# Kernel tuning notes

Hardware: AMD Instinct MI355X
Metric: run time of the kernel (lower is better)

The kernel has to match this reference:

```python
import jax, jax.numpy as jnp
import numpy as np
from jax import lax

B_, L_, D_ = 4, 2048, 256
DI, NS, DC, DTR = 512, 16, 4, 16  # d_inner=2*D, d_state, d_conv, dt_rank=ceil(D/16)
DFF = 4 * D_


def setup_inputs():
    key = jax.random.key(0)
    ks = jax.random.split(key, 20)
    rn = lambda k, s, sc=0.02: jax.random.normal(k, s, jnp.float32) * sc
    return {
        "x": jax.random.normal(ks[0], (B_, L_, D_), jnp.float32),
        "in_proj_w": rn(ks[1], (2 * DI, D_)), "in_proj_b": jnp.zeros((2 * DI,), jnp.float32),
        "conv_w": rn(ks[2], (DI, DC), 0.1), "conv_b": jnp.zeros((DI,), jnp.float32),
        "x_proj_w": rn(ks[3], (DTR + 2 * NS, DI)),
        "dt_proj_w": rn(ks[4], (DI, DTR), 0.1), "dt_proj_b": rn(ks[5], (DI,), 0.5),
        "A_log": jnp.log(jnp.tile(jnp.arange(1, NS + 1, dtype=jnp.float32), (DI, 1))),
        "D_ssm": jnp.ones((DI,), jnp.float32),
        "out_proj_w": rn(ks[6], (D_, DI)), "out_proj_b": jnp.zeros((D_,), jnp.float32),
        "ln1_g": jnp.ones((D_,), jnp.float32), "ln1_b": jnp.zeros((D_,), jnp.float32),
        "fc1_w": rn(ks[7], (DFF, D_)), "fc1_b": jnp.zeros((DFF,), jnp.float32),
        "fc2_w": rn(ks[8], (D_, DFF)), "fc2_b": jnp.zeros((D_,), jnp.float32),
        "ln2_g": jnp.ones((D_,), jnp.float32), "ln2_b": jnp.zeros((D_,), jnp.float32),
    }


def _layer_norm(x, g, b, eps=1e-5):
    m = jnp.mean(x, -1, keepdims=True)
    v = jnp.mean((x - m) ** 2, -1, keepdims=True)
    return (x - m) / jnp.sqrt(v + eps) * g + b


def _mamba(x, in_proj_w, in_proj_b, conv_w, conv_b, x_proj_w, dt_proj_w, dt_proj_b, A_log, D_ssm, out_proj_w, out_proj_b):
    B, L, D = x.shape
    xz = x @ in_proj_w.T + in_proj_b                       # [B,L,2*DI]
    xi, z = jnp.split(xz, 2, axis=-1)
    # causal depthwise conv over time
    xc = jnp.transpose(xi, (0, 2, 1))                       # [B,DI,L]
    xc = lax.conv_general_dilated(xc, conv_w[:, None, :], (1,), [(DC - 1, 0)],
                                  dimension_numbers=("NCH", "OIH", "NCH"),
                                  feature_group_count=DI)
    xi = jax.nn.silu(jnp.transpose(xc + conv_b[None, :, None], (0, 2, 1)))  # [B,L,DI]
    x_dbl = xi @ x_proj_w.T                                 # [B,L,DTR+2*NS]
    dt, Bs, Cs = jnp.split(x_dbl, [DTR, DTR + NS], axis=-1)
    dt = jax.nn.softplus(dt @ dt_proj_w.T + dt_proj_b)      # [B,L,DI]
    A = -jnp.exp(A_log)                                     # [DI,NS]
    dA = jnp.exp(dt[..., None] * A)                         # [B,L,DI,NS]
    dBu = dt[..., None] * Bs[:, :, None, :] * xi[..., None]  # [B,L,DI,NS]
    dA_t = jnp.moveaxis(dA, 1, 0)
    dBu_t = jnp.moveaxis(dBu, 1, 0)
    C_t = jnp.moveaxis(Cs, 1, 0)                            # [L,B,NS]

    def step(h, inp):
        a, bu, c = inp
        h = a * h + bu                                      # [B,DI,NS]
        y = jnp.einsum("bdn,bn->bd", h, c)
        return h, y

    h0 = jnp.zeros((B, DI, NS), x.dtype)
    _, ys = lax.scan(step, h0, (dA_t, dBu_t, C_t))
    y = jnp.moveaxis(ys, 0, 1) + xi * D_ssm                 # [B,L,DI]
    y = y * jax.nn.silu(z)
    return y @ out_proj_w.T + out_proj_b


def reference(x, in_proj_w, in_proj_b, conv_w, conv_b, x_proj_w, dt_proj_w, dt_proj_b,
              A_log, D_ssm, out_proj_w, out_proj_b, ln1_g, ln1_b, fc1_w, fc1_b,
              fc2_w, fc2_b, ln2_g, ln2_b):
    gelu = lambda t: jax.nn.gelu(t, approximate=False)
    ssm = _mamba(x, in_proj_w, in_proj_b, conv_w, conv_b, x_proj_w, dt_proj_w,
                 dt_proj_b, A_log, D_ssm, out_proj_w, out_proj_b)
    y = _layer_norm(x + ssm, ln1_g, ln1_b)                  # dropout = identity (eval)
    ffn = gelu(gelu(y @ fc1_w.T + fc1_b) @ fc2_w.T + fc2_b)
    return _layer_norm(y + ffn, ln2_g, ln2_b)
```

## Files before the change

kernel.cpp:

```cpp
#include <hip/hip_runtime.h>

typedef __bf16 bf16x8 __attribute__((ext_vector_type(8)));
typedef float  f32x4  __attribute__((ext_vector_type(4)));

#define AS1 __attribute__((address_space(1)))
#define AS3 __attribute__((address_space(3)))

__device__ __forceinline__ float bf2f(ushort u) {
    union { unsigned int i; float f; } v; v.i = ((unsigned int)u) << 16; return v.f;
}
__device__ __forceinline__ ushort f2bf(float f) {
    union { float f; unsigned int i; } v; v.f = f;
    unsigned int i = v.i;
    unsigned int r = i + 0x7FFFu + ((i >> 16) & 1u);
    return (ushort)(r >> 16);
}
__device__ __forceinline__ float bflo(unsigned int u) { return bf2f((ushort)(u & 0xFFFFu)); }
__device__ __forceinline__ float bfhi(unsigned int u) { return bf2f((ushort)(u >> 16)); }
__device__ __forceinline__ float gelu_f(float v) {
    return 0.5f * v * (1.f + erff(v * 0.70710678118654752f));
}

__device__ __forceinline__ bool sniff_inline(const ushort* __restrict__ x) {
    const int lane = threadIdx.x & 63;
    int cnt = 0;
    #pragma unroll
    for (int r = 0; r < 4; r++) {
        const ushort u = x[lane + r * 64];
        const int e = (u >> 7) & 0xFF;
        if ((u & 0x7FFF) == 0 || (e >= 112 && e <= 141)) cnt++;
    }
    #pragma unroll
    for (int o = 32; o > 0; o >>= 1) cnt += __shfl_xor(cnt, o);
    return cnt >= 224;
}

struct CanonArgs {
    const void* src[20];
    int off[20];
    int total;
};

__launch_bounds__(256)
__global__ void canon_k(CanonArgs a, ushort* __restrict__ dst, ushort* __restrict__ xpw_pad,
                        const ushort* __restrict__ sniffx)
{
    const int i = blockIdx.x * 256 + threadIdx.x;
    if (i >= a.total) {
        const int j = i - a.total;
        if (j < 8192) xpw_pad[24576 + j] = 0;
        return;
    }
    const bool fl = sniff_inline(sniffx);
    int s = 0;
    #pragma unroll
    for (int t = 1; t < 20; t++) if (i >= a.off[t]) s = t;
    const int li = i - a.off[s];
    ushort v;
    if (fl) v = ((const ushort*)a.src[s])[li];
    else    v = f2bf(((const float*)a.src[s])[li]);
    dst[i] = v;
    if (s == 5) xpw_pad[li] = v;
}

template<int BM, int BN>
__launch_bounds__(256, 2)
__global__ void gemm_bt(const ushort* __restrict__ A, const ushort* __restrict__ W,
                        const ushort* __restrict__ bias, ushort* __restrict__ Cb,
                        int N, int K)
{
    constexpr int WMT = BM / 32;
    constexpr int WNT = BN / 32;
    __shared__ __align__(16) ushort As[BM * 32];
    __shared__ __align__(16) ushort Bs[BN * 32];
    const int tid  = threadIdx.x;
    const int wave = tid >> 6;
    const int lane = tid & 63;
    const int m0 = blockIdx.x * BM;
    const int n0 = blockIdx.y * BN;
    const int wm = (wave >> 1) * (BM / 2);
    const int wn = (wave & 1) * (BN / 2);
    const int lrow = lane & 15;
    const int quad = lane >> 4;

    f32x4 acc[WMT][WNT];
    #pragma unroll
    for (int i = 0; i < WMT; i++)
        #pragma unroll
        for (int j = 0; j < WNT; j++)
            #pragma unroll
            for (int r = 0; r < 4; r++) acc[i][j][r] = 0.f;

    for (int k0 = 0; k0 < K; k0 += 32) {
        #pragma unroll
        for (int t = 0; t < BM / 64; t++) {
            const int inst = t * 4 + wave;
            const int row  = inst * 16 + (lane >> 2);
            const int sub  = lane & 3;
            const ushort* gp = A + (size_t)(m0 + row) * K + (k0 + sub * 8);
            __builtin_amdgcn_global_load_lds((AS1 void*)(void*)gp,
                                             (AS3 void*)(As + inst * 512), 16, 0, 0);
        }
        #pragma unroll
        for (int t = 0; t < BN / 64; t++) {
            const int inst = t * 4 + wave;
            const int row  = inst * 16 + (lane >> 2);
            const int sub  = lane & 3;
            const ushort* gp = W + (size_t)(n0 + row) * K + (k0 + sub * 8);
            __builtin_amdgcn_global_load_lds((AS1 void*)(void*)gp,
                                             (AS3 void*)(Bs + inst * 512), 16, 0, 0);
        }
        __syncthreads();
        bf16x8 afr[WMT], bfr[WNT];
        #pragma unroll
        for (int i = 0; i < WMT; i++)
            afr[i] = *(const bf16x8*)&As[(wm + i * 16 + lrow) * 32 + quad * 8];
        #pragma unroll
        for (int j = 0; j < WNT; j++)
            bfr[j] = *(const bf16x8*)&Bs[(wn + j * 16 + lrow) * 32 + quad * 8];
        #pragma unroll
        for (int i = 0; i < WMT; i++)
            #pragma unroll
            for (int j = 0; j < WNT; j++)
                acc[i][j] = __builtin_amdgcn_mfma_f32_16x16x32_bf16(afr[i], bfr[j], acc[i][j], 0, 0, 0);
        __syncthreads();
    }

    #pragma unroll
    for (int i = 0; i < WMT; i++) {
        const int gm = m0 + wm + i * 16 + quad * 4;
        #pragma unroll
        for (int j = 0; j < WNT; j++) {
            const int gn = n0 + wn + j * 16 + lrow;
            const float bv = bf2f(bias[gn]);
            #pragma unroll
            for (int r = 0; r < 4; r++)
                Cb[(size_t)(gm + r) * N + gn] = f2bf(acc[i][j][r] + bv);
        }
    }
}

__launch_bounds__(512)
__global__ void convscan1_k(const ushort* __restrict__ xz, const ushort* __restrict__ cw,
                            const ushort* __restrict__ cb, const ushort* __restrict__ xpw_pad,
                            const ushort* __restrict__ dtw, const ushort* __restrict__ dtb,
                            const ushort* __restrict__ Alog,
                            float* __restrict__ xdbl, float* __restrict__ summh,
                            float* __restrict__ sdtb)
{
    __shared__ __align__(16) ushort xcs[16 * 520];
    __shared__ float XD[16 * 48];
    const int tid  = threadIdx.x;
    const int wave = tid >> 6;
    const int lane = tid & 63;
    const int lrow = lane & 15;
    const int quad = lane >> 4;
    const int c = blockIdx.x, b = blockIdx.y;
    const int t0 = b * 2048 + c * 16;

    {
        const int d8 = (tid & 63) * 8;
        ushort wl[32];
        *(uint4*)&wl[0]  = *(const uint4*)&cw[d8 * 4];
        *(uint4*)&wl[8]  = *(const uint4*)&cw[d8 * 4 + 8];
        *(uint4*)&wl[16] = *(const uint4*)&cw[d8 * 4 + 16];
        *(uint4*)&wl[24] = *(const uint4*)&cw[d8 * 4 + 24];
        ushort bl[8];
        *(uint4*)&bl[0] = *(const uint4*)&cb[d8];
        #pragma unroll
        for (int it = 0; it < 2; it++) {
            const int trow = it * 8 + wave;
            const int t = t0 + trow;
            const int l = t & 2047;
            float acc[8];
            #pragma unroll
            for (int j = 0; j < 8; j++) acc[j] = bf2f(bl[j]);
            #pragma unroll
            for (int k = 0; k < 4; k++) {
                const int ls = l - 3 + k;
                if (ls >= 0) {
                    ushort xl[8];
                    *(uint4*)&xl[0] = *(const uint4*)&xz[(size_t)(t - 3 + k) * 1024 + d8];
                    #pragma unroll
                    for (int j = 0; j < 8; j++) acc[j] += bf2f(xl[j]) * bf2f(wl[j * 4 + k]);
                }
            }
            ushort ol[8];
            #pragma unroll
            for (int j = 0; j < 8; j++) {
                const float s = acc[j] / (1.f + __expf(-acc[j]));
                ol[j] = f2bf(s);
            }
            *(uint4*)&xcs[trow * 520 + d8] = *(uint4*)&ol[0];
        }
    }
    __syncthreads();

    if (wave < 3) {
        const int nt = wave;
        const ushort* bptr = xpw_pad + (size_t)(nt * 16 + lrow) * 512 + quad * 8;
        f32x4 acc = {0.f, 0.f, 0.f, 0.f};
        bf16x8 bn = *(const bf16x8*)bptr;
        for (int k0 = 0; k0 < 512; k0 += 32) {
            const bf16x8 bc = bn;
            if (k0 + 32 < 512) bn = *(const bf16x8*)(bptr + k0 + 32);
            const bf16x8 afr = *(const bf16x8*)&xcs[lrow * 520 + k0 + quad * 8];
            acc = __builtin_amdgcn_mfma_f32_16x16x32_bf16(afr, bc, acc, 0, 0, 0);
        }
        const int col = nt * 16 + lrow;
        #pragma unroll
        for (int r = 0; r < 4; r++) {
            const int row = quad * 4 + r;
            XD[row * 48 + col] = acc[r];
            xdbl[(size_t)(t0 + row) * 64 + col] = acc[r];
        }
    }
    __syncthreads();

    {
        const int d = tid;
        const uint4 w0 = *(const uint4*)&dtw[d * 16];
        const uint4 w1 = *(const uint4*)&dtw[d * 16 + 8];
        const float wd[16] = { bflo(w0.x), bfhi(w0.x), bflo(w0.y), bfhi(w0.y),
                               bflo(w0.z), bfhi(w0.z), bflo(w0.w), bfhi(w0.w),
                               bflo(w1.x), bfhi(w1.x), bflo(w1.y), bfhi(w1.y),
                               bflo(w1.z), bfhi(w1.z), bflo(w1.w), bfhi(w1.w) };
        const float dtbv = bf2f(dtb[d]);
        float A[16], h[16];
        #pragma unroll
        for (int n = 0; n < 16; n++) {
            A[n] = -__expf(bf2f(Alog[d * 16 + n]));
            h[n] = 0.f;
        }
        float sdt = 0.f;
        for (int i = 0; i < 16; i++) {
            const float* Xr = &XD[i * 48];
            float s = dtbv;
            #pragma unroll
            for (int k = 0; k < 16; k++) s += Xr[k] * wd[k];
            const float dtv = (s > 15.f) ? s : __logf(1.f + __expf(s));
            const float xiv = bf2f(xcs[i * 520 + d]);
            const float dx = dtv * xiv;
            sdt += dtv;
            #pragma unroll
            for (int n = 0; n < 16; n++) {
                const float da = __expf(dtv * A[n]);
                h[n] = da * h[n] + dx * Xr[16 + n];
            }
        }
        const size_t bh = ((size_t)(b * 128 + c) * 16) * 512 + d;
        #pragma unroll
        for (int n = 0; n < 16; n++) summh[bh + (size_t)n * 512] = h[n];
        sdtb[(size_t)(b * 128 + c) * 512 + d] = sdt;
    }
}

__launch_bounds__(512)
__global__ void combine_k(float* __restrict__ summh, const float* __restrict__ sdtb,
                          const ushort* __restrict__ Alog)
{
    const int b = blockIdx.x >> 4, n = blockIdx.x & 15;
    const int d = threadIdx.x;
    const float An = -__expf(bf2f(Alog[d * 16 + n]));
    float h = 0.f;
    #pragma unroll
    for (int q = 0; q < 4; q++) {
        float p[32], hl[32], ho[32];
        #pragma unroll
        for (int c2 = 0; c2 < 32; c2++) {
            const int cc = q * 32 + c2;
            hl[c2] = summh[((size_t)(b * 128 + cc) * 16 + n) * 512 + d];
            p[c2]  = __expf(An * sdtb[(size_t)(b * 128 + cc) * 512 + d]);
        }
        #pragma unroll
        for (int c2 = 0; c2 < 32; c2++) {
            ho[c2] = h;
            h = p[c2] * h + hl[c2];
        }
        #pragma unroll
        for (int c2 = 0; c2 < 32; c2++)
            summh[((size_t)(b * 128 + (q * 32 + c2)) * 16 + n) * 512 + d] = ho[c2];
    }
}

__launch_bounds__(512)
__global__ void tail_k(const ushort* __restrict__ xz, const ushort* __restrict__ cw,
                       const ushort* __restrict__ cb, const float* __restrict__ xdbl,
                       const ushort* __restrict__ dtw, const ushort* __restrict__ dtb,
                       const ushort* __restrict__ Alog, const float* __restrict__ summh,
                       const ushort* __restrict__ Dssm, const ushort* __restrict__ cx,
                       const ushort* __restrict__ opw, const ushort* __restrict__ opb,
                       const ushort* __restrict__ ln1g, const ushort* __restrict__ ln1b,
                       const ushort* __restrict__ f1w, const ushort* __restrict__ f1b,
                       const ushort* __restrict__ f2w, const ushort* __restrict__ f2b,
                       const ushort* __restrict__ ln2g, const ushort* __restrict__ ln2b,
                       void* __restrict__ dout, const ushort* __restrict__ sniffx)
{
    __shared__ __align__(16) ushort yls[16 * 520];
    __shared__ float XD[16 * 48];
    __shared__ __align__(16) ushort y1bs[16 * 264];
    __shared__ float redS[8 * 16], redQ[8 * 16];
    ushort* f1q = yls;

    const int tid  = threadIdx.x;
    const int wave = tid >> 6;
    const int lane = tid & 63;
    const int lrow = lane & 15;
    const int quad = lane >> 4;
    const int c = blockIdx.x, b = blockIdx.y;
    const int t0 = b * 2048 + c * 16;
    const int n0w = wave * 32;

    {
        const int d8 = (tid & 63) * 8;
        ushort wl[32];
        *(uint4*)&wl[0]  = *(const uint4*)&cw[d8 * 4];
        *(uint4*)&wl[8]  = *(const uint4*)&cw[d8 * 4 + 8];
        *(uint4*)&wl[16] = *(const uint4*)&cw[d8 * 4 + 16];
        *(uint4*)&wl[24] = *(const uint4*)&cw[d8 * 4 + 24];
        ushort bl[8];
        *(uint4*)&bl[0] = *(const uint4*)&cb[d8];
        #pragma unroll
        for (int it = 0; it < 2; it++) {
            const int trow = it * 8 + wave;
            const int t = t0 + trow;
            const int l = t & 2047;
            float acc[8];
            #pragma unroll
            for (int j = 0; j < 8; j++) acc[j] = bf2f(bl[j]);
            #pragma unroll
            for (int k = 0; k < 4; k++) {
                const int ls = l - 3 + k;
                if (ls >= 0) {
                    ushort xl[8];
                    *(uint4*)&xl[0] = *(const uint4*)&xz[(size_t)(t - 3 + k) * 1024 + d8];
                    #pragma unroll
                    for (int j = 0; j < 8; j++) acc[j] += bf2f(xl[j]) * bf2f(wl[j * 4 + k]);
                }
            }
            ushort ol[8];
            #pragma unroll
            for (int j = 0; j < 8; j++) {
                const float s = acc[j] / (1.f + __expf(-acc[j]));
                ol[j] = f2bf(s);
            }
            *(uint4*)&yls[trow * 520 + d8] = *(uint4*)&ol[0];
        }
    }
    for (int e = tid; e < 768; e += 512)
        XD[e] = xdbl[(size_t)(t0 + (e / 48)) * 64 + (e % 48)];
    __syncthreads();

    {
        const int d = tid;
        const uint4 w0 = *(const uint4*)&dtw[d * 16];
        const uint4 w1 = *(const uint4*)&dtw[d * 16 + 8];
        const float wd[16] = { bflo(w0.x), bfhi(w0.x), bflo(w0.y), bfhi(w0.y),
                               bflo(w0.z), bfhi(w0.z), bflo(w0.w), bfhi(w0.w),
                               bflo(w1.x), bfhi(w1.x), bflo(w1.y), bfhi(w1.y),
                               bflo(w1.z), bfhi(w1.z), bflo(w1.w), bfhi(w1.w) };
        const float dtbv = bf2f(dtb[d]);
        float A[16], h[16];
        #pragma unroll
        for (int n = 0; n < 16; n++) A[n] = -__expf(bf2f(Alog[d * 16 + n]));
        const size_t bh = ((size_t)(b * 128 + c) * 16) * 512 + d;
        #pragma unroll
        for (int n = 0; n < 16; n++) h[n] = summh[bh + (size_t)n * 512];
        const float Dv = bf2f(Dssm[d]);
        for (int i = 0; i < 16; i++) {
            const int t = t0 + i;
            const float* Xr = &XD[i * 48];
            float s = dtbv;
            #pragma unroll
            for (int k = 0; k < 16; k++) s += Xr[k] * wd[k];
            const float dtv = (s > 15.f) ? s : __logf(1.f + __expf(s));
            const float xiv = bf2f(yls[i * 520 + d]);
            const float dx = dtv * xiv;
            float yv = 0.f;
            #pragma unroll
            for (int n = 0; n < 16; n++) {
                const float da = __expf(dtv * A[n]);
                h[n] = da * h[n] + dx * Xr[16 + n];
                yv += h[n] * Xr[32 + n];
            }
            yv += xiv * Dv;
            const float zv = bf2f(xz[(size_t)t * 1024 + 512 + d]);
            yv *= zv / (1.f + __expf(-zv));
            yls[i * 520 + d] = f2bf(yv);
        }
    }
    __syncthreads();

    f32x4 accP[2];
    #pragma unroll
    for (int j = 0; j < 2; j++)
        #pragma unroll
        for (int r = 0; r < 4; r++) accP[j][r] = 0.f;
    {
        const ushort* bp0 = opw + (size_t)(n0w + lrow) * 512 + quad * 8;
        const ushort* bp1 = opw + (size_t)(n0w + 16 + lrow) * 512 + quad * 8;
        bf16x8 bn0 = *(const bf16x8*)bp0;
        bf16x8 bn1 = *(const bf16x8*)bp1;
        for (int k0 = 0; k0 < 512; k0 += 32) {
            const bf16x8 bc0 = bn0, bc1 = bn1;
            if (k0 + 32 < 512) {
                bn0 = *(const bf16x8*)(bp0 + k0 + 32);
                bn1 = *(const bf16x8*)(bp1 + k0 + 32);
            }
            const bf16x8 afr = *(const bf16x8*)&yls[lrow * 520 + k0 + quad * 8];
            accP[0] = __builtin_amdgcn_mfma_f32_16x16x32_bf16(afr, bc0, accP[0], 0, 0, 0);
            accP[1] = __builtin_amdgcn_mfma_f32_16x16x32_bf16(afr, bc1, accP[1], 0, 0, 0);
        }
    }
    float vP[2][4];
    float ps[4], pq[4];
    #pragma unroll
    for (int r = 0; r < 4; r++) { ps[r] = 0.f; pq[r] = 0.f; }
    #pragma unroll
    for (int j = 0; j < 2; j++) {
        const int col = n0w + j * 16 + lrow;
        const float bv = bf2f(opb[col]);
        #pragma unroll
        for (int r = 0; r < 4; r++) {
            const int row = quad * 4 + r;
            float v = accP[j][r] + bv + bf2f(cx[(size_t)(t0 + row) * 256 + col]);
            vP[j][r] = v;
            ps[r] += v;
            pq[r] += v * v;
        }
    }
    #pragma unroll
    for (int r = 0; r < 4; r++) {
        #pragma unroll
        for (int o = 8; o > 0; o >>= 1) {
            ps[r] += __shfl_xor(ps[r], o);
            pq[r] += __shfl_xor(pq[r], o);
        }
        if (lrow == 0) {
            const int row = quad * 4 + r;
            redS[wave * 16 + row] = ps[r];
            redQ[wave * 16 + row] = pq[r];
        }
    }
    __syncthreads();

    float y1f[2][4];
    #pragma unroll
    for (int r = 0; r < 4; r++) {
        const int row = quad * 4 + r;
        float S = 0.f, Q = 0.f;
        #pragma unroll
        for (int w = 0; w < 8; w++) { S += redS[w * 16 + row]; Q += redQ[w * 16 + row]; }
        const float mean = S * (1.f / 256.f);
        const float var  = Q * (1.f / 256.f) - mean * mean;
        const float rs   = rsqrtf(var + 1e-5f);
        #pragma unroll
        for (int j = 0; j < 2; j++) {
            const int col = n0w + j * 16 + lrow;
            const float o2 = (vP[j][r] - mean) * rs * bf2f(ln1g[col]) + bf2f(ln1b[col]);
            y1f[j][r] = o2;
            y1bs[row * 264 + col] = f2bf(o2);
        }
    }
    __syncthreads();

    f32x4 acc2[2];
    #pragma unroll
    for (int j = 0; j < 2; j++)
        #pragma unroll
        for (int r = 0; r < 4; r++) acc2[j][r] = 0.f;

    for (int q = 0; q < 4; q++) {
        f32x4 a1[2];
        #pragma unroll
        for (int j = 0; j < 2; j++)
            #pragma unroll
            for (int r = 0; r < 4; r++) a1[j][r] = 0.f;
        {
            const ushort* bp0 = f1w + (size_t)(q * 256 + n0w + lrow) * 256 + quad * 8;
            const ushort* bp1 = f1w + (size_t)(q * 256 + n0w + 16 + lrow) * 256 + quad * 8;
            bf16x8 bn0 = *(const bf16x8*)bp0;
            bf16x8 bn1 = *(const bf16x8*)bp1;
            for (int k0 = 0; k0 < 256; k0 += 32) {
                const bf16x8 bc0 = bn0, bc1 = bn1;
                if (k0 + 32 < 256) {
                    bn0 = *(const bf16x8*)(bp0 + k0 + 32);
                    bn1 = *(const bf16x8*)(bp1 + k0 + 32);
                }
                const bf16x8 afr = *(const bf16x8*)&y1bs[lrow * 264 + k0 + quad * 8];
                a1[0] = __builtin_amdgcn_mfma_f32_16x16x32_bf16(afr, bc0, a1[0], 0, 0, 0);
                a1[1] = __builtin_amdgcn_mfma_f32_16x16x32_bf16(afr, bc1, a1[1], 0, 0, 0);
            }
        }
        #pragma unroll
        for (int j = 0; j < 2; j++) {
            const int qc = n0w + j * 16 + lrow;
            const float bv = bf2f(f1b[q * 256 + qc]);
            #pragma unroll
            for (int r = 0; r < 4; r++) {
                const int row = quad * 4 + r;
                f1q[row * 260 + qc] = f2bf(gelu_f(a1[j][r] + bv));
            }
        }
        __syncthreads();
        {
            const ushort* bp0 = f2w + (size_t)(n0w + lrow) * 1024 + q * 256 + quad * 8;
            const ushort* bp1 = f2w + (size_t)(n0w + 16 + lrow) * 1024 + q * 256 + quad * 8;
            bf16x8 bn0 = *(const bf16x8*)bp0;
            bf16x8 bn1 = *(const bf16x8*)bp1;
            for (int k0 = 0; k0 < 256; k0 += 32) {
                const bf16x8 bc0 = bn0, bc1 = bn1;
                if (k0 + 32 < 256) {
                    bn0 = *(const bf16x8*)(bp0 + k0 + 32);
                    bn1 = *(const bf16x8*)(bp1 + k0 + 32);
                }
                const bf16x8 afr = *(const bf16x8*)&f1q[lrow * 260 + k0 + quad * 8];
                acc2[0] = __builtin_amdgcn_mfma_f32_16x16x32_bf16(afr, bc0, acc2[0], 0, 0, 0);
                acc2[1] = __builtin_amdgcn_mfma_f32_16x16x32_bf16(afr, bc1, acc2[1], 0, 0, 0);
            }
        }
        __syncthreads();
    }

    float v2[2][4];
    #pragma unroll
    for (int r = 0; r < 4; r++) { ps[r] = 0.f; pq[r] = 0.f; }
    #pragma unroll
    for (int j = 0; j < 2; j++) {
        const int col = n0w + j * 16 + lrow;
        const float bv = bf2f(f2b[col]);
        #pragma unroll
        for (int r = 0; r < 4; r++) {
            const float v = gelu_f(acc2[j][r] + bv) + y1f[j][r];
            v2[j][r] = v;
            ps[r] += v;
            pq[r] += v * v;
        }
    }
    #pragma unroll
    for (int r = 0; r < 4; r++) {
        #pragma unroll
        for (int o = 8; o > 0; o >>= 1) {
            ps[r] += __shfl_xor(ps[r], o);
            pq[r] += __shfl_xor(pq[r], o);
        }
        if (lrow == 0) {
            const int row = quad * 4 + r;
            redS[wave * 16 + row] = ps[r];
            redQ[wave * 16 + row] = pq[r];
        }
    }
    __syncthreads();

    const bool fl = sniff_inline(sniffx);
    #pragma unroll
    for (int r = 0; r < 4; r++) {
        const int row = quad * 4 + r;
        float S = 0.f, Q = 0.f;
        #pragma unroll
        for (int w = 0; w < 8; w++) { S += redS[w * 16 + row]; Q += redQ[w * 16 + row]; }
        const float mean = S * (1.f / 256.f);
        const float var  = Q * (1.f / 256.f) - mean * mean;
        const float rs   = rsqrtf(var + 1e-5f);
        #pragma unroll
        for (int j = 0; j < 2; j++) {
            const int col = n0w + j * 16 + lrow;
            const size_t off = (size_t)(t0 + row) * 256 + col;
            const float o2 = (v2[j][r] - mean) * rs * bf2f(ln2g[col]) + bf2f(ln2b[col]);
            if (fl) ((ushort*)dout)[off] = f2bf(o2);
            else    ((float*)dout)[off]  = o2;
        }
    }
}

extern "C" void kernel_launch(void* const* d_in, const int* in_sizes, int n_in,
                              void* d_out, int out_size, void* d_ws, size_t ws_size,
                              hipStream_t stream)
{
    char* ws = (char*)d_ws;
    ushort* canon = (ushort*)(ws + 256);

    static const int coff[20] = {
        0,        2097152,  2359296,  2360320,  2362368,
        2362880,  2387456,  2395648,  2396160,  2404352,
        2404864,  2535936,  2536192,  2536448,  2536704,
        2798848,  2799872,  3062016,  3062272,  3062528 };
    static const int ctot = 3062784;

    CanonArgs ca;
    for (int i = 0; i < 20; i++) { ca.src[i] = d_in[i]; ca.off[i] = coff[i]; }
    ca.total = ctot;

    const ushort* cx   = canon + coff[0];
    const ushort* cipw = canon + coff[1];
    const ushort* cipb = canon + coff[2];
    const ushort* ccw  = canon + coff[3];
    const ushort* ccb  = canon + coff[4];
    const ushort* cdtw = canon + coff[6];
    const ushort* cdtb = canon + coff[7];
    const ushort* calog= canon + coff[8];
    const ushort* cdssm= canon + coff[9];
    const ushort* copw = canon + coff[10];
    const ushort* copb = canon + coff[11];
    const ushort* cln1g= canon + coff[12];
    const ushort* cln1b= canon + coff[13];
    const ushort* cf1w = canon + coff[14];
    const ushort* cf1b = canon + coff[15];
    const ushort* cf2w = canon + coff[16];
    const ushort* cf2b = canon + coff[17];
    const ushort* cln2g= canon + coff[18];
    const ushort* cln2b= canon + coff[19];

    ushort* xpw_pad = (ushort*)(ws + 6291456);
    ushort* xz      = (ushort*)(ws + 8388608);
    float*  xdbl    = (float*)(ws + 25165824);
    float*  summh   = (float*)(ws + 27262976);
    float*  sdtb    = (float*)(ws + 44040192);
    const ushort* sx = (const ushort*)d_in[0];

    canon_k<<<(ctot + 8192 + 255) / 256, 256, 0, stream>>>(ca, canon, xpw_pad, sx);
    gemm_bt<128, 128><<<dim3(64, 8), 256, 0, stream>>>(cx, cipw, cipb, xz, 1024, 256);
    convscan1_k<<<dim3(128, 4), 512, 0, stream>>>(
        xz, ccw, ccb, xpw_pad, cdtw, cdtb, calog, xdbl, summh, sdtb);
    combine_k<<<64, 512, 0, stream>>>(summh, sdtb, calog);
    tail_k<<<dim3(128, 4), 512, 0, stream>>>(
        xz, ccw, ccb, xdbl, cdtw, cdtb, calog, summh, cdssm, cx,
        copw, copb, cln1g, cln1b, cf1w, cf1b, cf2w, cf2b, cln2g, cln2b,
        d_out, sx);
}
```

Before: 258.8 us.

## Use 32-step scan chunks with half-chunk states and split combine across threads

```diff
diff --git a/kernel.cpp b/kernel.cpp
--- a/kernel.cpp
+++ b/kernel.cpp
@@ -146,17 +146,18 @@
                             const ushort* __restrict__ dtw, const ushort* __restrict__ dtb,
                             const ushort* __restrict__ Alog,
                             float* __restrict__ xdbl, float* __restrict__ summh,
-                            float* __restrict__ sdtb)
+                            float* __restrict__ sdt32, float* __restrict__ hhalf,
+                            float* __restrict__ sdthalf)
 {
-    __shared__ __align__(16) ushort xcs[16 * 520];
-    __shared__ float XD[16 * 48];
+    __shared__ __align__(16) ushort xcs[32 * 520];
+    __shared__ float XD[32 * 48];
     const int tid  = threadIdx.x;
     const int wave = tid >> 6;
     const int lane = tid & 63;
     const int lrow = lane & 15;
     const int quad = lane >> 4;
     const int c = blockIdx.x, b = blockIdx.y;
-    const int t0 = b * 2048 + c * 16;
+    const int t0 = b * 2048 + c * 32;
 
     {
         const int d8 = (tid & 63) * 8;
@@ -168,7 +169,7 @@
         ushort bl[8];
         *(uint4*)&bl[0] = *(const uint4*)&cb[d8];
         #pragma unroll
-        for (int it = 0; it < 2; it++) {
+        for (int it = 0; it < 4; it++) {
             const int trow = it * 8 + wave;
             const int t = t0 + trow;
             const int l = t & 2047;
@@ -196,23 +197,30 @@
     }
     __syncthreads();
 
-    if (wave < 3) {
-        const int nt = wave;
+    {
+        const int mt = wave >> 2, nt = wave & 3;
         const ushort* bptr = xpw_pad + (size_t)(nt * 16 + lrow) * 512 + quad * 8;
         f32x4 acc = {0.f, 0.f, 0.f, 0.f};
-        bf16x8 bn = *(const bf16x8*)bptr;
-        for (int k0 = 0; k0 < 512; k0 += 32) {
-            const bf16x8 bc = bn;
-            if (k0 + 32 < 512) bn = *(const bf16x8*)(bptr + k0 + 32);
-            const bf16x8 afr = *(const bf16x8*)&xcs[lrow * 520 + k0 + quad * 8];
-            acc = __builtin_amdgcn_mfma_f32_16x16x32_bf16(afr, bc, acc, 0, 0, 0);
+        #pragma unroll
+        for (int hh = 0; hh < 2; hh++) {
+            bf16x8 Bv[8];
+            #pragma unroll
+            for (int s = 0; s < 8; s++)
+                Bv[s] = *(const bf16x8*)(bptr + hh * 256 + s * 32);
+            #pragma unroll
+            for (int s = 0; s < 8; s++) {
+                const bf16x8 afr = *(const bf16x8*)&xcs[(mt * 16 + lrow) * 520 + hh * 256 + s * 32 + quad * 8];
+                acc = __builtin_amdgcn_mfma_f32_16x16x32_bf16(afr, Bv[s], acc, 0, 0, 0);
+            }
         }
         const int col = nt * 16 + lrow;
-        #pragma unroll
-        for (int r = 0; r < 4; r++) {
-            const int row = quad * 4 + r;
-            XD[row * 48 + col] = acc[r];
-            xdbl[(size_t)(t0 + row) * 64 + col] = acc[r];
+        if (col < 48) {
+            #pragma unroll
+            for (int r = 0; r < 4; r++) {
+                const int row = mt * 16 + quad * 4 + r;
+                XD[row * 48 + col] = acc[r];
+                xdbl[(size_t)(t0 + row) * 64 + col] = acc[r];
+            }
         }
     }
     __syncthreads();
@@ -232,12 +240,20 @@
             A[n] = -__expf(bf2f(Alog[d * 16 + n]));
             h[n] = 0.f;
         }
+        const size_t bh = ((size_t)(b * 64 + c) * 16) * 512 + d;
+        const size_t bs = (size_t)(b * 64 + c) * 512 + d;
         float sdt = 0.f;
-        for (int i = 0; i < 16; i++) {
+        for (int i = 0; i < 32; i++) {
             const float* Xr = &XD[i * 48];
-            float s = dtbv;
-            #pragma unroll
-            for (int k = 0; k < 16; k++) s += Xr[k] * wd[k];
+            float s0 = dtbv, s1 = 0.f, s2 = 0.f, s3 = 0.f;
+            #pragma unroll
+            for (int k = 0; k < 16; k += 4) {
+                s0 += Xr[k]     * wd[k];
+                s1 += Xr[k + 1] * wd[k + 1];
+                s2 += Xr[k + 2] * wd[k + 2];
+                s3 += Xr[k + 3] * wd[k + 3];
+            }
+            const float s = (s0 + s1) + (s2 + s3);
             const float dtv = (s > 15.f) ? s : __logf(1.f + __expf(s));
             const float xiv = bf2f(xcs[i * 520 + d]);
             const float dx = dtv * xiv;
@@ -247,30 +263,36 @@
                 const float da = __expf(dtv * A[n]);
                 h[n] = da * h[n] + dx * Xr[16 + n];
             }
-        }
-        const size_t bh = ((size_t)(b * 128 + c) * 16) * 512 + d;
+            if (i == 15) {
+                #pragma unroll
+                for (int n = 0; n < 16; n++) hhalf[bh + (size_t)n * 512] = h[n];
+                sdthalf[bs] = sdt;
+            }
+        }
         #pragma unroll
         for (int n = 0; n < 16; n++) summh[bh + (size_t)n * 512] = h[n];
-        sdtb[(size_t)(b * 128 + c) * 512 + d] = sdt;
-    }
-}
-
-__launch_bounds__(512)
-__global__ void combine_k(float* __restrict__ summh, const float* __restrict__ sdtb,
+        sdt32[bs] = sdt;
+    }
+}
+
+__launch_bounds__(128)
+__global__ void combine_k(float* __restrict__ summh, const float* __restrict__ sdt32,
                           const ushort* __restrict__ Alog)
 {
-    const int b = blockIdx.x >> 4, n = blockIdx.x & 15;
-    const int d = threadIdx.x;
+    const int b  = blockIdx.x >> 6;
+    const int n  = (blockIdx.x >> 2) & 15;
+    const int dq = blockIdx.x & 3;
+    const int d  = dq * 128 + threadIdx.x;
     const float An = -__expf(bf2f(Alog[d * 16 + n]));
     float h = 0.f;
     #pragma unroll
-    for (int q = 0; q < 4; q++) {
+    for (int q = 0; q < 2; q++) {
         float p[32], hl[32], ho[32];
         #pragma unroll
         for (int c2 = 0; c2 < 32; c2++) {
             const int cc = q * 32 + c2;
-            hl[c2] = summh[((size_t)(b * 128 + cc) * 16 + n) * 512 + d];
-            p[c2]  = __expf(An * sdtb[(size_t)(b * 128 + cc) * 512 + d]);
+            hl[c2] = summh[((size_t)(b * 64 + cc) * 16 + n) * 512 + d];
+            p[c2]  = __expf(An * sdt32[(size_t)(b * 64 + cc) * 512 + d]);
         }
         #pragma unroll
         for (int c2 = 0; c2 < 32; c2++) {
@@ -279,15 +301,16 @@
         }
         #pragma unroll
         for (int c2 = 0; c2 < 32; c2++)
-            summh[((size_t)(b * 128 + (q * 32 + c2)) * 16 + n) * 512 + d] = ho[c2];
-    }
-}
-
-__launch_bounds__(512)
+            summh[((size_t)(b * 64 + (q * 32 + c2)) * 16 + n) * 512 + d] = ho[c2];
+    }
+}
+
+__launch_bounds__(512, 4)
 __global__ void tail_k(const ushort* __restrict__ xz, const ushort* __restrict__ cw,
                        const ushort* __restrict__ cb, const float* __restrict__ xdbl,
                        const ushort* __restrict__ dtw, const ushort* __restrict__ dtb,
                        const ushort* __restrict__ Alog, const float* __restrict__ summh,
+                       const float* __restrict__ hhalf, const float* __restrict__ sdthalf,
                        const ushort* __restrict__ Dssm, const ushort* __restrict__ cx,
                        const ushort* __restrict__ opw, const ushort* __restrict__ opb,
                        const ushort* __restrict__ ln1g, const ushort* __restrict__ ln1b,
@@ -363,26 +386,43 @@
         float A[16], h[16];
         #pragma unroll
         for (int n = 0; n < 16; n++) A[n] = -__expf(bf2f(Alog[d * 16 + n]));
-        const size_t bh = ((size_t)(b * 128 + c) * 16) * 512 + d;
+        const int c32 = c >> 1;
+        const size_t bh = ((size_t)(b * 64 + c32) * 16) * 512 + d;
         #pragma unroll
         for (int n = 0; n < 16; n++) h[n] = summh[bh + (size_t)n * 512];
+        if (c & 1) {
+            const float sdth = sdthalf[(size_t)(b * 64 + c32) * 512 + d];
+            #pragma unroll
+            for (int n = 0; n < 16; n++)
+                h[n] = __expf(A[n] * sdth) * h[n] + hhalf[bh + (size_t)n * 512];
+        }
         const float Dv = bf2f(Dssm[d]);
         for (int i = 0; i < 16; i++) {
             const int t = t0 + i;
             const float* Xr = &XD[i * 48];
-            float s = dtbv;
-            #pragma unroll
-            for (int k = 0; k < 16; k++) s += Xr[k] * wd[k];
+            float s0 = dtbv, s1 = 0.f, s2 = 0.f, s3 = 0.f;
+            #pragma unroll
+            for (int k = 0; k < 16; k += 4) {
+                s0 += Xr[k]     * wd[k];
+                s1 += Xr[k + 1] * wd[k + 1];
+                s2 += Xr[k + 2] * wd[k + 2];
+                s3 += Xr[k + 3] * wd[k + 3];
+            }
+            const float s = (s0 + s1) + (s2 + s3);
             const float dtv = (s > 15.f) ? s : __logf(1.f + __expf(s));
             const float xiv = bf2f(yls[i * 520 + d]);
             const float dx = dtv * xiv;
-            float yv = 0.f;
-            #pragma unroll
-            for (int n = 0; n < 16; n++) {
-                const float da = __expf(dtv * A[n]);
-                h[n] = da * h[n] + dx * Xr[16 + n];
-                yv += h[n] * Xr[32 + n];
-            }
+            float yv0 = 0.f, yv1 = 0.f;
+            #pragma unroll
+            for (int n = 0; n < 16; n += 2) {
+                const float da0 = __expf(dtv * A[n]);
+                const float da1 = __expf(dtv * A[n + 1]);
+                h[n]     = da0 * h[n]     + dx * Xr[16 + n];
+                h[n + 1] = da1 * h[n + 1] + dx * Xr[17 + n];
+                yv0 += h[n]     * Xr[32 + n];
+                yv1 += h[n + 1] * Xr[33 + n];
+            }
+            float yv = yv0 + yv1;
             yv += xiv * Dv;
             const float zv = bf2f(xz[(size_t)t * 1024 + 512 + d]);
             yv *= zv / (1.f + __expf(-zv));
@@ -399,17 +439,20 @@
     {
         const ushort* bp0 = opw + (size_t)(n0w + lrow) * 512 + quad * 8;
         const ushort* bp1 = opw + (size_t)(n0w + 16 + lrow) * 512 + quad * 8;
-        bf16x8 bn0 = *(const bf16x8*)bp0;
-        bf16x8 bn1 = *(const bf16x8*)bp1;
-        for (int k0 = 0; k0 < 512; k0 += 32) {
-            const bf16x8 bc0 = bn0, bc1 = bn1;
-            if (k0 + 32 < 512) {
-                bn0 = *(const bf16x8*)(bp0 + k0 + 32);
-                bn1 = *(const bf16x8*)(bp1 + k0 + 32);
-            }
-            const bf16x8 afr = *(const bf16x8*)&yls[lrow * 520 + k0 + quad * 8];
-            accP[0] = __builtin_amdgcn_mfma_f32_16x16x32_bf16(afr, bc0, accP[0], 0, 0, 0);
-            accP[1] = __builtin_amdgcn_mfma_f32_16x16x32_bf16(afr, bc1, accP[1], 0, 0, 0);
+        #pragma unroll
+        for (int hh = 0; hh < 2; hh++) {
+            bf16x8 B0[8], B1[8];
+            #pragma unroll
+            for (int s = 0; s < 8; s++) {
+                B0[s] = *(const bf16x8*)(bp0 + hh * 256 + s * 32);
+                B1[s] = *(const bf16x8*)(bp1 + hh * 256 + s * 32);
+            }
+            #pragma unroll
+            for (int s = 0; s < 8; s++) {
+                const bf16x8 afr = *(const bf16x8*)&yls[lrow * 520 + hh * 256 + s * 32 + quad * 8];
+                accP[0] = __builtin_amdgcn_mfma_f32_16x16x32_bf16(afr, B0[s], accP[0], 0, 0, 0);
+                accP[1] = __builtin_amdgcn_mfma_f32_16x16x32_bf16(afr, B1[s], accP[1], 0, 0, 0);
+            }
         }
     }
     float vP[2][4];
@@ -479,17 +522,17 @@
         {
             const ushort* bp0 = f1w + (size_t)(q * 256 + n0w + lrow) * 256 + quad * 8;
             const ushort* bp1 = f1w + (size_t)(q * 256 + n0w + 16 + lrow) * 256 + quad * 8;
-            bf16x8 bn0 = *(const bf16x8*)bp0;
-            bf16x8 bn1 = *(const bf16x8*)bp1;
-            for (int k0 = 0; k0 < 256; k0 += 32) {
-                const bf16x8 bc0 = bn0, bc1 = bn1;
-                if (k0 + 32 < 256) {
-                    bn0 = *(const bf16x8*)(bp0 + k0 + 32);
-                    bn1 = *(const bf16x8*)(bp1 + k0 + 32);
-                }
-                const bf16x8 afr = *(const bf16x8*)&y1bs[lrow * 264 + k0 + quad * 8];
-                a1[0] = __builtin_amdgcn_mfma_f32_16x16x32_bf16(afr, bc0, a1[0], 0, 0, 0);
-                a1[1] = __builtin_amdgcn_mfma_f32_16x16x32_bf16(afr, bc1, a1[1], 0, 0, 0);
+            bf16x8 B0[8], B1[8];
+            #pragma unroll
+            for (int s = 0; s < 8; s++) {
+                B0[s] = *(const bf16x8*)(bp0 + s * 32);
+                B1[s] = *(const bf16x8*)(bp1 + s * 32);
+            }
+            #pragma unroll
+            for (int s = 0; s < 8; s++) {
+                const bf16x8 afr = *(const bf16x8*)&y1bs[lrow * 264 + s * 32 + quad * 8];
+                a1[0] = __builtin_amdgcn_mfma_f32_16x16x32_bf16(afr, B0[s], a1[0], 0, 0, 0);
+                a1[1] = __builtin_amdgcn_mfma_f32_16x16x32_bf16(afr, B1[s], a1[1], 0, 0, 0);
             }
         }
         #pragma unroll
@@ -506,17 +549,17 @@
         {
             const ushort* bp0 = f2w + (size_t)(n0w + lrow) * 1024 + q * 256 + quad * 8;
             const ushort* bp1 = f2w + (size_t)(n0w + 16 + lrow) * 1024 + q * 256 + quad * 8;
-            bf16x8 bn0 = *(const bf16x8*)bp0;
-            bf16x8 bn1 = *(const bf16x8*)bp1;
-            for (int k0 = 0; k0 < 256; k0 += 32) {
-                const bf16x8 bc0 = bn0, bc1 = bn1;
-                if (k0 + 32 < 256) {
-                    bn0 = *(const bf16x8*)(bp0 + k0 + 32);
-                    bn1 = *(const bf16x8*)(bp1 + k0 + 32);
-                }
-                const bf16x8 afr = *(const bf16x8*)&f1q[lrow * 260 + k0 + quad * 8];
-                acc2[0] = __builtin_amdgcn_mfma_f32_16x16x32_bf16(afr, bc0, acc2[0], 0, 0, 0);
-                acc2[1] = __builtin_amdgcn_mfma_f32_16x16x32_bf16(afr, bc1, acc2[1], 0, 0, 0);
+            bf16x8 B0[8], B1[8];
+            #pragma unroll
+            for (int s = 0; s < 8; s++) {
+                B0[s] = *(const bf16x8*)(bp0 + s * 32);
+                B1[s] = *(const bf16x8*)(bp1 + s * 32);
+            }
+            #pragma unroll
+            for (int s = 0; s < 8; s++) {
+                const bf16x8 afr = *(const bf16x8*)&f1q[lrow * 260 + s * 32 + quad * 8];
+                acc2[0] = __builtin_amdgcn_mfma_f32_16x16x32_bf16(afr, B0[s], acc2[0], 0, 0, 0);
+                acc2[1] = __builtin_amdgcn_mfma_f32_16x16x32_bf16(afr, B1[s], acc2[1], 0, 0, 0);
             }
         }
         __syncthreads();
@@ -615,16 +658,18 @@
     ushort* xz      = (ushort*)(ws + 8388608);
     float*  xdbl    = (float*)(ws + 25165824);
     float*  summh   = (float*)(ws + 27262976);
-    float*  sdtb    = (float*)(ws + 44040192);
+    float*  hhalf   = (float*)(ws + 35651584);
+    float*  sdt32   = (float*)(ws + 44040192);
+    float*  sdthalf = (float*)(ws + 44564480);
     const ushort* sx = (const ushort*)d_in[0];
 
     canon_k<<<(ctot + 8192 + 255) / 256, 256, 0, stream>>>(ca, canon, xpw_pad, sx);
     gemm_bt<128, 128><<<dim3(64, 8), 256, 0, stream>>>(cx, cipw, cipb, xz, 1024, 256);
-    convscan1_k<<<dim3(128, 4), 512, 0, stream>>>(
-        xz, ccw, ccb, xpw_pad, cdtw, cdtb, calog, xdbl, summh, sdtb);
-    combine_k<<<64, 512, 0, stream>>>(summh, sdtb, calog);
+    convscan1_k<<<dim3(64, 4), 512, 0, stream>>>(
+        xz, ccw, ccb, xpw_pad, cdtw, cdtb, calog, xdbl, summh, sdt32, hhalf, sdthalf);
+    combine_k<<<256, 128, 0, stream>>>(summh, sdt32, calog);
     tail_k<<<dim3(128, 4), 512, 0, stream>>>(
-        xz, ccw, ccb, xdbl, cdtw, cdtb, calog, summh, cdssm, cx,
+        xz, ccw, ccb, xdbl, cdtw, cdtb, calog, summh, hhalf, sdthalf, cdssm, cx,
         copw, copb, cln1g, cln1b, cf1w, cf1b, cf2w, cf2b, cln2g, cln2b,
         d_out, sx);
 }
```

After: 255.5 us. No clear change (-1.3%).
